# Optimization experiments

Measured on AMD Instinct MI355X. Metric: run time of the kernel, lower is better.

Reference implementation:

```python
import jax, jax.numpy as jnp
import numpy as np

B, N, D = 4, 2048, 768
OUT = 768

def setup_inputs() -> dict:
    key = jax.random.key(0)
    k1, k2 = jax.random.split(key)
    x = jax.random.normal(k1, (B, N, D), dtype=jnp.float32)
    kernel = jax.random.normal(k2, (3, D, OUT), dtype=jnp.float32) * 0.02
    return {"x": x, "kernel": kernel}

def reference(x, kernel):
    # Single-head attention with shared QKV kernel stack [3, D, OUT]
    q = jnp.einsum('bnd,do->bno', x, kernel[0])
    k = jnp.einsum('bnd,do->bno', x, kernel[1])
    v = jnp.einsum('bnd,do->bno', x, kernel[2])
    # NOTE: original divides by 64**0.5 == 8 regardless of dims (faithful)
    scores = jnp.einsum('bqo,bko->bqk', q, k) / 8.0
    attn = jax.nn.softmax(scores, axis=-1)
    return jnp.einsum('bqk,bko->bqo', attn, v)
```

## Files before the change

kernel.cpp:

```cpp
#include <hip/hip_runtime.h>
#include <hip/hip_bf16.h>

constexpr int B_ = 4, N_ = 2048, D_ = 768, OUT_ = 768;
constexpr int M_ = B_ * N_;

typedef __attribute__((ext_vector_type(8))) short short8;
typedef __attribute__((ext_vector_type(4))) float floatx4;

__device__ __forceinline__ unsigned short f2bfu(float f) {
    union { __hip_bfloat16 b; unsigned short u; } cv;
    cv.b = __float2bfloat16(f);
    return cv.u;
}

#define GLOAD_LDS16(g, l)                                                     \
    __builtin_amdgcn_global_load_lds(                                         \
        (const __attribute__((address_space(1))) void*)(g),                   \
        (__attribute__((address_space(3))) void*)(l), 16, 0, 0)

template <int NT>
__device__ __forceinline__ void gemm256_core(
    const __hip_bfloat16* __restrict__ aG, int lda,
    const __hip_bfloat16* __restrict__ bG, int ldb,
    unsigned short* LDS, floatx4 (&acc)[8][4]) {
    const int tid = threadIdx.x;
    const int wave = tid >> 6, lane = tid & 63;
    const int lrow = lane & 15, kq = lane >> 4;
    const int wm = (wave >> 2) * 128, wn = (wave & 3) * 64;

    const __hip_bfloat16* sA[2];
    const __hip_bfloat16* sB[2];
#pragma unroll
    for (int i = 0; i < 2; ++i) {
        const int u = i * 512 + tid;
        const int p = u >> 3, g = (u & 7) ^ (p & 7);
        const int row = 2 * p + (g >> 2), ch = g & 3;
        sA[i] = aG + (size_t)row * lda + ch * 8;
        sB[i] = bG + (size_t)row * ldb + ch * 8;
    }
    int offA[8], offB[4];
#pragma unroll
    for (int mi = 0; mi < 8; ++mi) {
        const int row = wm + mi * 16 + lrow;
        const int p = row >> 1, g = ((row & 1) << 2) | kq;
        offA[mi] = p * 64 + ((g ^ (p & 7)) * 8);
    }
#pragma unroll
    for (int ni = 0; ni < 4; ++ni) {
        const int row = wn + ni * 16 + lrow;
        const int p = row >> 1, g = ((row & 1) << 2) | kq;
        offB[ni] = p * 64 + ((g ^ (p & 7)) * 8);
    }

#define STAGE_T(ti)                                                        \
    do {                                                                   \
        unsigned short* dst_ = LDS + ((ti) & 3) * 16384 + wave * 512;      \
        GLOAD_LDS16(sA[0], dst_);                                          \
        GLOAD_LDS16(sA[1], dst_ + 4096);                                   \
        GLOAD_LDS16(sB[0], dst_ + 8192);                                   \
        GLOAD_LDS16(sB[1], dst_ + 12288);                                  \
        sA[0] += 32; sA[1] += 32; sB[0] += 32; sB[1] += 32;                \
    } while (0)

    STAGE_T(0);
    STAGE_T(1);
    STAGE_T(2);
    asm volatile("s_waitcnt vmcnt(8)" ::: "memory");
    __builtin_amdgcn_s_barrier();
    __builtin_amdgcn_sched_barrier(0);

    for (int t = 0; t < NT; ++t) {
        if (t + 3 < NT) STAGE_T(t + 3);
        const unsigned short* Sa = LDS + (t & 3) * 16384;
        const unsigned short* Sb = Sa + 8192;
        short8 bf[4], af[8];
#pragma unroll
        for (int ni = 0; ni < 4; ++ni)
            bf[ni] = *(const short8*)(Sb + offB[ni]);
#pragma unroll
        for (int mi = 0; mi < 8; ++mi)
            af[mi] = *(const short8*)(Sa + offA[mi]);
        __builtin_amdgcn_s_setprio(1);
#pragma unroll
        for (int mi = 0; mi < 8; ++mi)
#pragma unroll
            for (int ni = 0; ni < 4; ++ni)
                acc[mi][ni] = __builtin_amdgcn_mfma_f32_16x16x32_bf16(
                    af[mi], bf[ni], acc[mi][ni], 0, 0, 0);
        __builtin_amdgcn_s_setprio(0);
        if (t + 3 < NT) {
            asm volatile("s_waitcnt vmcnt(8)" ::: "memory");
        } else if (t + 2 < NT) {
            asm volatile("s_waitcnt vmcnt(4)" ::: "memory");
        } else if (t + 1 < NT) {
            asm volatile("s_waitcnt vmcnt(0)" ::: "memory");
        }
        if (t + 1 < NT) {
            __builtin_amdgcn_s_barrier();
            __builtin_amdgcn_sched_barrier(0);
        }
    }
#undef STAGE_T
}

__global__ __launch_bounds__(256)
void prep(const float* __restrict__ x, const float* __restrict__ w,
          __hip_bfloat16* __restrict__ xb, __hip_bfloat16* __restrict__ wt,
          float* __restrict__ l, float* __restrict__ out) {
    __shared__ float t[32][33];
    const int tid = threadIdx.x;
    if (blockIdx.x < 3072) {
        const size_t i = (size_t)blockIdx.x * 2048 + (size_t)tid * 8;
        float4 a = *(const float4*)(x + i);
        float4 b = *(const float4*)(x + i + 4);
        *(ushort4*)((unsigned short*)xb + i) =
            make_ushort4(f2bfu(a.x), f2bfu(a.y), f2bfu(a.z), f2bfu(a.w));
        *(ushort4*)((unsigned short*)xb + i + 4) =
            make_ushort4(f2bfu(b.x), f2bfu(b.y), f2bfu(b.z), f2bfu(b.w));
    } else if (blockIdx.x < 4800) {
        const int bid = blockIdx.x - 3072;
        const int s = bid / 576, rem = bid % 576;
        const int d0 = (rem / 24) * 32, o0 = (rem % 24) * 32;
        const int tx = tid & 31, ty = tid >> 5;
        const float* ws = w + (size_t)s * D_ * OUT_;
        __hip_bfloat16* wts = wt + (size_t)s * OUT_ * D_;
#pragma unroll
        for (int i = 0; i < 4; ++i)
            t[ty + 8 * i][tx] = ws[(size_t)(d0 + ty + 8 * i) * OUT_ + o0 + tx];
        __syncthreads();
#pragma unroll
        for (int i = 0; i < 4; ++i)
            wts[(size_t)(o0 + ty + 8 * i) * D_ + d0 + tx] =
                __float2bfloat16(t[tx][ty + 8 * i]);
    } else if (blockIdx.x == 4800) {
        float4* l4 = (float4*)l;
#pragma unroll
        for (int i = 0; i < 8; ++i) l4[i * 256 + tid] = make_float4(0, 0, 0, 0);
    } else {
        const size_t bid2 = blockIdx.x - 4801;
        ((float4*)out)[bid2 * 256 + tid] = make_float4(0, 0, 0, 0);
    }
}

__global__ __launch_bounds__(512, 2)
void qkv_mfma(const __hip_bfloat16* __restrict__ xb,
              const __hip_bfloat16* __restrict__ wt,
              __hip_bfloat16* __restrict__ q, __hip_bfloat16* __restrict__ k,
              __hip_bfloat16* __restrict__ vt) {
    __shared__ __align__(16) unsigned short LDS[65536];
    const int s = blockIdx.z;
    const int m0 = blockIdx.x * 256, n0 = blockIdx.y * 256;
    floatx4 acc[8][4] = {};
    gemm256_core<24>(xb + (size_t)m0 * D_, D_,
                     wt + (size_t)s * OUT_ * D_ + (size_t)n0 * D_, D_, LDS,
                     acc);

    const int tid = threadIdx.x, wave = tid >> 6, lane = tid & 63;
    const int lrow = lane & 15, kq = lane >> 4;
    const int wm = (wave >> 2) * 128, wn = (wave & 3) * 64;

    if (s < 2) {
        unsigned short* outp = (unsigned short*)(s == 0 ? q : k);
#pragma unroll
        for (int mi = 0; mi < 8; ++mi)
#pragma unroll
            for (int r = 0; r < 4; ++r) {
                const size_t ro =
                    (size_t)(m0 + wm + mi * 16 + kq * 4 + r) * OUT_ + n0 + wn;
#pragma unroll
                for (int ni = 0; ni < 4; ++ni)
                    outp[ro + ni * 16 + lrow] = f2bfu(acc[mi][ni][r]);
            }
    } else {
        unsigned short* E = LDS;
        const int b = m0 >> 11, j0 = m0 & 2047;
#pragma unroll
        for (int h = 0; h < 2; ++h) {
            __syncthreads();
            if ((wave >> 2) == h) {
#pragma unroll
                for (int ni = 0; ni < 4; ++ni)
#pragma unroll
                    for (int mi = 0; mi < 8; ++mi)
#pragma unroll
                        for (int r = 0; r < 4; ++r)
                            E[(wn + ni * 16 + lrow) * 136 + mi * 16 + kq * 4 +
                              r] = f2bfu(acc[mi][ni][r]);
            }
            __syncthreads();
#pragma unroll
            for (int i = 0; i < 8; ++i) {
                const int u = i * 512 + tid, nr = u >> 4, c = u & 15;
                short8 vv = *(const short8*)(E + nr * 136 + c * 8);
                *(short8*)((unsigned short*)vt +
                           ((size_t)b * OUT_ + n0 + nr) * N_ + j0 + h * 128 +
                           c * 8) = vv;
            }
        }
    }
}

__global__ __launch_bounds__(512, 2)
void scores_mfma(const __hip_bfloat16* __restrict__ q,
                 const __hip_bfloat16* __restrict__ k,
                 __hip_bfloat16* __restrict__ pt, float* __restrict__ l) {
    __shared__ __align__(16) unsigned short LDS[65536];
    const int b = blockIdx.z;
    const int m0 = blockIdx.x * 256, n0 = blockIdx.y * 256;
    floatx4 acc[8][4] = {};
    gemm256_core<24>(q + (size_t)b * N_ * OUT_ + (size_t)m0 * OUT_, OUT_,
                     k + (size_t)b * N_ * OUT_ + (size_t)n0 * OUT_, OUT_, LDS,
                     acc);

    const int tid = threadIdx.x, wave = tid >> 6, lane = tid & 63;
    const int lrow = lane & 15, kq = lane >> 4;
    const int wm = (wave >> 2) * 128, wn = (wave & 3) * 64;

    float rs[8][4];
#pragma unroll
    for (int mi = 0; mi < 8; ++mi)
#pragma unroll
        for (int r = 0; r < 4; ++r) rs[mi][r] = 0.0f;
#pragma unroll
    for (int mi = 0; mi < 8; ++mi)
#pragma unroll
        for (int ni = 0; ni < 4; ++ni)
#pragma unroll
            for (int r = 0; r < 4; ++r) {
                const float e = __expf(acc[mi][ni][r] * 0.125f - 8.0f);
                acc[mi][ni][r] = e;
                rs[mi][r] += e;
            }
#pragma unroll
    for (int mi = 0; mi < 8; ++mi)
#pragma unroll
        for (int r = 0; r < 4; ++r) {
            float v = rs[mi][r];
            v += __shfl_xor(v, 1, 64);
            v += __shfl_xor(v, 2, 64);
            v += __shfl_xor(v, 4, 64);
            v += __shfl_xor(v, 8, 64);
            if (lrow == 0)
                atomicAdd(&l[(size_t)b * N_ + m0 + wm + mi * 16 + kq * 4 + r],
                          v);
        }
    unsigned short* pb = (unsigned short*)pt + (size_t)b * N_ * N_;
#pragma unroll
    for (int mi = 0; mi < 8; ++mi)
#pragma unroll
        for (int r = 0; r < 4; ++r) {
            const size_t ro =
                (size_t)(m0 + wm + mi * 16 + kq * 4 + r) * N_ + n0 + wn;
#pragma unroll
            for (int ni = 0; ni < 4; ++ni)
                pb[ro + ni * 16 + lrow] = f2bfu(acc[mi][ni][r]);
        }
}

__global__ __launch_bounds__(512, 2)
void pv_mfma(const __hip_bfloat16* __restrict__ pt,
             const __hip_bfloat16* __restrict__ vt,
             const float* __restrict__ l, float* __restrict__ out) {
    __shared__ __align__(16) unsigned short LDS[65536];
    const int b = blockIdx.z >> 1, h = blockIdx.z & 1;
    const int m0 = blockIdx.x * 256, n0 = blockIdx.y * 256;
    floatx4 acc[8][4] = {};
    gemm256_core<32>(
        pt + (size_t)b * N_ * N_ + (size_t)m0 * N_ + h * 1024, N_,
        vt + (size_t)b * OUT_ * N_ + (size_t)n0 * N_ + h * 1024, N_, LDS, acc);

    const int tid = threadIdx.x, wave = tid >> 6, lane = tid & 63;
    const int lrow = lane & 15, kq = lane >> 4;
    const int wm = (wave >> 2) * 128, wn = (wave & 3) * 64;
    const float* lb = l + (size_t)b * N_ + m0 + wm;
#pragma unroll
    for (int mi = 0; mi < 8; ++mi)
#pragma unroll
        for (int r = 0; r < 4; ++r) {
            const float inv = 1.0f / lb[mi * 16 + kq * 4 + r];
            float* o = out +
                       ((size_t)b * N_ + m0 + wm + mi * 16 + kq * 4 + r) *
                           OUT_ +
                       n0 + wn;
#pragma unroll
            for (int ni = 0; ni < 4; ++ni)
                atomicAdd(o + ni * 16 + lrow, acc[mi][ni][r] * inv);
        }
}

extern "C" void kernel_launch(void* const* d_in, const int* in_sizes, int n_in,
                              void* d_out, int out_size, void* d_ws,
                              size_t ws_size, hipStream_t stream) {
    const float* x = (const float*)d_in[0];
    const float* w = (const float*)d_in[1];
    float* out = (float*)d_out;

    __hip_bfloat16* q  = (__hip_bfloat16*)d_ws;
    __hip_bfloat16* k  = q + (size_t)M_ * OUT_;
    __hip_bfloat16* vt = k + (size_t)M_ * OUT_;
    __hip_bfloat16* xb = vt + (size_t)M_ * OUT_;
    __hip_bfloat16* wt = xb + (size_t)M_ * D_;
    float* l = (float*)(wt + (size_t)3 * OUT_ * D_);
    __hip_bfloat16* pt = (__hip_bfloat16*)(l + M_);

    prep<<<dim3(10945), dim3(256), 0, stream>>>(x, w, xb, wt, l, out);
    qkv_mfma<<<dim3(32, 3, 3), dim3(512), 0, stream>>>(xb, wt, q, k, vt);
    scores_mfma<<<dim3(8, 8, 4), dim3(512), 0, stream>>>(q, k, pt, l);
    pv_mfma<<<dim3(8, 3, 8), dim3(512), 0, stream>>>(pt, vt, l, out);
}
```

Baseline: 227.5 us.

## Restructure GEMM pipelines with 64-wide K double-buffering and smaller M tiles

Replaces the shared 256x256 GEMM core with two variants that stage a 64-wide K step in two halves with double buffering: a 256x256 version for scores and a 128x256 version for the QKV and PV products. The 128x256 tile doubles the block count for QKV and PV. PV no longer splits K, so its output is written with plain stores instead of atomics and the output-zeroing pass in prep is removed. Q/K and score epilogues are staged through LDS to produce 16-byte coalesced stores. The price is more barriers per K step and a different LDS footprint.

```diff
diff --git a/kernel.cpp b/kernel.cpp
--- a/kernel.cpp
+++ b/kernel.cpp
@@ -18,95 +18,236 @@
         (const __attribute__((address_space(1))) void*)(g),                   \
         (__attribute__((address_space(3))) void*)(l), 16, 0, 0)
 
+#define MFMA_BF16 __builtin_amdgcn_mfma_f32_16x16x32_bf16
+#define WAIT_LGKM0 asm volatile("s_waitcnt lgkmcnt(0)" ::: "memory")
+
+
 template <int NT>
-__device__ __forceinline__ void gemm256_core(
+__device__ __forceinline__ void gemm4p(
     const __hip_bfloat16* __restrict__ aG, int lda,
     const __hip_bfloat16* __restrict__ bG, int ldb,
     unsigned short* LDS, floatx4 (&acc)[8][4]) {
+    constexpr int ASLOT = 8192, BSLOT = 8192, BUFS = 32768;
     const int tid = threadIdx.x;
     const int wave = tid >> 6, lane = tid & 63;
     const int lrow = lane & 15, kq = lane >> 4;
     const int wm = (wave >> 2) * 128, wn = (wave & 3) * 64;
 
-    const __hip_bfloat16* sA[2];
-    const __hip_bfloat16* sB[2];
-#pragma unroll
-    for (int i = 0; i < 2; ++i) {
-        const int u = i * 512 + tid;
-        const int p = u >> 3, g = (u & 7) ^ (p & 7);
-        const int row = 2 * p + (g >> 2), ch = g & 3;
-        sA[i] = aG + (size_t)row * lda + ch * 8;
-        sB[i] = bG + (size_t)row * ldb + ch * 8;
-    }
-    int offA[8], offB[4];
-#pragma unroll
-    for (int mi = 0; mi < 8; ++mi) {
-        const int row = wm + mi * 16 + lrow;
-        const int p = row >> 1, g = ((row & 1) << 2) | kq;
-        offA[mi] = p * 64 + ((g ^ (p & 7)) * 8);
-    }
-#pragma unroll
-    for (int ni = 0; ni < 4; ++ni) {
-        const int row = wn + ni * 16 + lrow;
-        const int p = row >> 1, g = ((row & 1) << 2) | kq;
-        offB[ni] = p * 64 + ((g ^ (p & 7)) * 8);
-    }
-
-#define STAGE_T(ti)                                                        \
-    do {                                                                   \
-        unsigned short* dst_ = LDS + ((ti) & 3) * 16384 + wave * 512;      \
-        GLOAD_LDS16(sA[0], dst_);                                          \
-        GLOAD_LDS16(sA[1], dst_ + 4096);                                   \
-        GLOAD_LDS16(sB[0], dst_ + 8192);                                   \
-        GLOAD_LDS16(sB[1], dst_ + 12288);                                  \
-        sA[0] += 32; sA[1] += 32; sB[0] += 32; sB[1] += 32;                \
+    const __hip_bfloat16 *sa0, *sa1, *sb0, *sb1;
+    {
+        const int r0 = tid >> 2, g0 = (tid & 3) ^ (r0 & 3);
+        sa0 = aG + (size_t)r0 * lda + g0 * 8;
+        sb0 = bG + (size_t)r0 * ldb + g0 * 8;
+        const int u1 = 512 + tid, r1 = u1 >> 2, g1 = (u1 & 3) ^ (r1 & 3);
+        sa1 = aG + (size_t)r1 * lda + g1 * 8;
+        sb1 = bG + (size_t)r1 * ldb + g1 * 8;
+    }
+    int oa[8], ob[4];
+#pragma unroll
+    for (int i = 0; i < 8; ++i) {
+        const int r = wm + i * 16 + lrow;
+        oa[i] = r * 32 + ((kq ^ (r & 3)) * 8);
+    }
+#pragma unroll
+    for (int i = 0; i < 4; ++i) {
+        const int r = wn + i * 16 + lrow;
+        ob[i] = r * 32 + ((kq ^ (r & 3)) * 8);
+    }
+
+#define SA4(tt, kh)                                                          \
+    do {                                                                     \
+        unsigned short* d_ =                                                 \
+            LDS + ((tt) & 1) * BUFS + (kh) * ASLOT + wave * 512;             \
+        GLOAD_LDS16(sa0 + (tt) * 64 + (kh) * 32, d_);                        \
+        GLOAD_LDS16(sa1 + (tt) * 64 + (kh) * 32, d_ + 4096);                 \
     } while (0)
-
-    STAGE_T(0);
-    STAGE_T(1);
-    STAGE_T(2);
-    asm volatile("s_waitcnt vmcnt(8)" ::: "memory");
+#define SB4(tt, kh)                                                          \
+    do {                                                                     \
+        unsigned short* d_ = LDS + ((tt) & 1) * BUFS + 2 * ASLOT +           \
+                             (kh) * BSLOT + wave * 512;                      \
+        GLOAD_LDS16(sb0 + (tt) * 64 + (kh) * 32, d_);                        \
+        GLOAD_LDS16(sb1 + (tt) * 64 + (kh) * 32, d_ + 4096);                 \
+    } while (0)
+
+    SA4(0, 0); SB4(0, 0); SA4(0, 1); SB4(0, 1);
+    SA4(1, 0); SB4(1, 0); SA4(1, 1);
+    asm volatile("s_waitcnt vmcnt(6)" ::: "memory");
     __builtin_amdgcn_s_barrier();
     __builtin_amdgcn_sched_barrier(0);
 
     for (int t = 0; t < NT; ++t) {
-        if (t + 3 < NT) STAGE_T(t + 3);
-        const unsigned short* Sa = LDS + (t & 3) * 16384;
-        const unsigned short* Sb = Sa + 8192;
-        short8 bf[4], af[8];
-#pragma unroll
-        for (int ni = 0; ni < 4; ++ni)
-            bf[ni] = *(const short8*)(Sb + offB[ni]);
-#pragma unroll
-        for (int mi = 0; mi < 8; ++mi)
-            af[mi] = *(const short8*)(Sa + offA[mi]);
-        __builtin_amdgcn_s_setprio(1);
-#pragma unroll
-        for (int mi = 0; mi < 8; ++mi)
+        const unsigned short* Ab = LDS + (t & 1) * BUFS;
+        const unsigned short* Bb = Ab + 2 * ASLOT;
+        short8 af[8], bf0, bf1;
+#pragma unroll
+        for (int i = 0; i < 8; ++i) af[i] = *(const short8*)(Ab + oa[i]);
+        bf0 = *(const short8*)(Bb + ob[0]);
+        bf1 = *(const short8*)(Bb + ob[1]);
+        if (t + 1 < NT) SB4(t + 1, 1);
+        __builtin_amdgcn_s_barrier();
+        WAIT_LGKM0;
+        __builtin_amdgcn_sched_barrier(0);
+        __builtin_amdgcn_s_setprio(1);
+#pragma unroll
+        for (int mi = 0; mi < 8; ++mi) {
+            acc[mi][0] = MFMA_BF16(af[mi], bf0, acc[mi][0], 0, 0, 0);
+            acc[mi][1] = MFMA_BF16(af[mi], bf1, acc[mi][1], 0, 0, 0);
+        }
+        __builtin_amdgcn_s_setprio(0);
+        __builtin_amdgcn_s_barrier();
+        bf0 = *(const short8*)(Bb + ob[2]);
+        bf1 = *(const short8*)(Bb + ob[3]);
+        if (t + 2 < NT) SA4(t + 2, 0);
+        __builtin_amdgcn_s_barrier();
+        WAIT_LGKM0;
+        __builtin_amdgcn_sched_barrier(0);
+        __builtin_amdgcn_s_setprio(1);
+#pragma unroll
+        for (int mi = 0; mi < 8; ++mi) {
+            acc[mi][2] = MFMA_BF16(af[mi], bf0, acc[mi][2], 0, 0, 0);
+            acc[mi][3] = MFMA_BF16(af[mi], bf1, acc[mi][3], 0, 0, 0);
+        }
+        __builtin_amdgcn_s_setprio(0);
+        __builtin_amdgcn_s_barrier();
+#pragma unroll
+        for (int i = 0; i < 8; ++i)
+            af[i] = *(const short8*)(Ab + ASLOT + oa[i]);
+        bf0 = *(const short8*)(Bb + BSLOT + ob[2]);
+        bf1 = *(const short8*)(Bb + BSLOT + ob[3]);
+        if (t + 2 < NT) SB4(t + 2, 0);
+        __builtin_amdgcn_s_barrier();
+        WAIT_LGKM0;
+        __builtin_amdgcn_sched_barrier(0);
+        __builtin_amdgcn_s_setprio(1);
+#pragma unroll
+        for (int mi = 0; mi < 8; ++mi) {
+            acc[mi][2] = MFMA_BF16(af[mi], bf0, acc[mi][2], 0, 0, 0);
+            acc[mi][3] = MFMA_BF16(af[mi], bf1, acc[mi][3], 0, 0, 0);
+        }
+        __builtin_amdgcn_s_setprio(0);
+        __builtin_amdgcn_s_barrier();
+        bf0 = *(const short8*)(Bb + BSLOT + ob[0]);
+        bf1 = *(const short8*)(Bb + BSLOT + ob[1]);
+        if (t + 2 < NT) SA4(t + 2, 1);
+        __builtin_amdgcn_s_barrier();
+        WAIT_LGKM0;
+        __builtin_amdgcn_sched_barrier(0);
+        __builtin_amdgcn_s_setprio(1);
+#pragma unroll
+        for (int mi = 0; mi < 8; ++mi) {
+            acc[mi][0] = MFMA_BF16(af[mi], bf0, acc[mi][0], 0, 0, 0);
+            acc[mi][1] = MFMA_BF16(af[mi], bf1, acc[mi][1], 0, 0, 0);
+        }
+        __builtin_amdgcn_s_setprio(0);
+        if (t + 2 < NT)
+            asm volatile("s_waitcnt vmcnt(6)" ::: "memory");
+        else if (t + 1 < NT)
+            asm volatile("s_waitcnt vmcnt(0)" ::: "memory");
+        __builtin_amdgcn_s_barrier();
+        __builtin_amdgcn_sched_barrier(0);
+    }
+#undef SA4
+#undef SB4
+}
+
+template <int NT>
+__device__ __forceinline__ void gemm2p(
+    const __hip_bfloat16* __restrict__ aG, int lda,
+    const __hip_bfloat16* __restrict__ bG, int ldb,
+    unsigned short* LDS, floatx4 (&acc)[4][4]) {
+    constexpr int ASLOT = 4096, BSLOT = 8192, BUFS = 24576;
+    const int tid = threadIdx.x;
+    const int wave = tid >> 6, lane = tid & 63;
+    const int lrow = lane & 15, kq = lane >> 4;
+    const int wm = (wave >> 2) * 64, wn = (wave & 3) * 64;
+
+    const __hip_bfloat16 *sa0, *sb0, *sb1;
+    {
+        const int r0 = tid >> 2, g0 = (tid & 3) ^ (r0 & 3);
+        sa0 = aG + (size_t)r0 * lda + g0 * 8;
+        sb0 = bG + (size_t)r0 * ldb + g0 * 8;
+        const int u1 = 512 + tid, r1 = u1 >> 2, g1 = (u1 & 3) ^ (r1 & 3);
+        sb1 = bG + (size_t)r1 * ldb + g1 * 8;
+    }
+    int oa[4], ob[4];
+#pragma unroll
+    for (int i = 0; i < 4; ++i) {
+        const int ra = wm + i * 16 + lrow;
+        oa[i] = ra * 32 + ((kq ^ (ra & 3)) * 8);
+        const int rb = wn + i * 16 + lrow;
+        ob[i] = rb * 32 + ((kq ^ (rb & 3)) * 8);
+    }
+
+#define SA2(tt, kh)                                                          \
+    GLOAD_LDS16(sa0 + (tt) * 64 + (kh) * 32,                                 \
+                LDS + ((tt) & 1) * BUFS + (kh) * ASLOT + wave * 512)
+#define SB2(tt, kh)                                                          \
+    do {                                                                     \
+        unsigned short* d_ = LDS + ((tt) & 1) * BUFS + 2 * ASLOT +           \
+                             (kh) * BSLOT + wave * 512;                      \
+        GLOAD_LDS16(sb0 + (tt) * 64 + (kh) * 32, d_);                        \
+        GLOAD_LDS16(sb1 + (tt) * 64 + (kh) * 32, d_ + 4096);                 \
+    } while (0)
+
+    SA2(0, 0); SB2(0, 0);
+    SA2(0, 1); SB2(0, 1);
+    SA2(1, 0); SB2(1, 0);
+    asm volatile("s_waitcnt vmcnt(3)" ::: "memory");
+    __builtin_amdgcn_s_barrier();
+    __builtin_amdgcn_sched_barrier(0);
+
+    for (int t = 0; t < NT; ++t) {
+        const unsigned short* Ab = LDS + (t & 1) * BUFS;
+        const unsigned short* Bb = Ab + 2 * ASLOT;
+        short8 af[4], bf[4];
+#pragma unroll
+        for (int i = 0; i < 4; ++i) af[i] = *(const short8*)(Ab + oa[i]);
+#pragma unroll
+        for (int i = 0; i < 4; ++i) bf[i] = *(const short8*)(Bb + ob[i]);
+        if (t + 1 < NT) { SA2(t + 1, 1); SB2(t + 1, 1); }
+        __builtin_amdgcn_s_barrier();
+        WAIT_LGKM0;
+        __builtin_amdgcn_sched_barrier(0);
+        __builtin_amdgcn_s_setprio(1);
+#pragma unroll
+        for (int mi = 0; mi < 4; ++mi)
 #pragma unroll
             for (int ni = 0; ni < 4; ++ni)
-                acc[mi][ni] = __builtin_amdgcn_mfma_f32_16x16x32_bf16(
-                    af[mi], bf[ni], acc[mi][ni], 0, 0, 0);
-        __builtin_amdgcn_s_setprio(0);
-        if (t + 3 < NT) {
-            asm volatile("s_waitcnt vmcnt(8)" ::: "memory");
-        } else if (t + 2 < NT) {
-            asm volatile("s_waitcnt vmcnt(4)" ::: "memory");
-        } else if (t + 1 < NT) {
+                acc[mi][ni] = MFMA_BF16(af[mi], bf[ni], acc[mi][ni], 0, 0, 0);
+        __builtin_amdgcn_s_setprio(0);
+        __builtin_amdgcn_s_barrier();
+#pragma unroll
+        for (int i = 0; i < 4; ++i)
+            af[i] = *(const short8*)(Ab + ASLOT + oa[i]);
+#pragma unroll
+        for (int i = 0; i < 4; ++i)
+            bf[i] = *(const short8*)(Bb + BSLOT + ob[i]);
+        if (t + 2 < NT) { SA2(t + 2, 0); SB2(t + 2, 0); }
+        __builtin_amdgcn_s_barrier();
+        WAIT_LGKM0;
+        __builtin_amdgcn_sched_barrier(0);
+        __builtin_amdgcn_s_setprio(1);
+#pragma unroll
+        for (int mi = 0; mi < 4; ++mi)
+#pragma unroll
+            for (int ni = 0; ni < 4; ++ni)
+                acc[mi][ni] = MFMA_BF16(af[mi], bf[ni], acc[mi][ni], 0, 0, 0);
+        __builtin_amdgcn_s_setprio(0);
+        if (t + 2 < NT)
+            asm volatile("s_waitcnt vmcnt(3)" ::: "memory");
+        else if (t + 1 < NT)
             asm volatile("s_waitcnt vmcnt(0)" ::: "memory");
-        }
-        if (t + 1 < NT) {
-            __builtin_amdgcn_s_barrier();
-            __builtin_amdgcn_sched_barrier(0);
-        }
-    }
-#undef STAGE_T
+        __builtin_amdgcn_s_barrier();
+        __builtin_amdgcn_sched_barrier(0);
+    }
+#undef SA2
+#undef SB2
 }
 
 __global__ __launch_bounds__(256)
 void prep(const float* __restrict__ x, const float* __restrict__ w,
           __hip_bfloat16* __restrict__ xb, __hip_bfloat16* __restrict__ wt,
-          float* __restrict__ l, float* __restrict__ out) {
+          float* __restrict__ l) {
     __shared__ float t[32][33];
     const int tid = threadIdx.x;
     if (blockIdx.x < 3072) {
@@ -132,13 +273,10 @@
         for (int i = 0; i < 4; ++i)
             wts[(size_t)(o0 + ty + 8 * i) * D_ + d0 + tx] =
                 __float2bfloat16(t[tx][ty + 8 * i]);
-    } else if (blockIdx.x == 4800) {
+    } else {
         float4* l4 = (float4*)l;
 #pragma unroll
         for (int i = 0; i < 8; ++i) l4[i * 256 + tid] = make_float4(0, 0, 0, 0);
-    } else {
-        const size_t bid2 = blockIdx.x - 4801;
-        ((float4*)out)[bid2 * 256 + tid] = make_float4(0, 0, 0, 0);
     }
 }
 
@@ -147,55 +285,57 @@
               const __hip_bfloat16* __restrict__ wt,
               __hip_bfloat16* __restrict__ q, __hip_bfloat16* __restrict__ k,
               __hip_bfloat16* __restrict__ vt) {
-    __shared__ __align__(16) unsigned short LDS[65536];
+    __shared__ __align__(16) unsigned short LDS[49152];
     const int s = blockIdx.z;
-    const int m0 = blockIdx.x * 256, n0 = blockIdx.y * 256;
-    floatx4 acc[8][4] = {};
-    gemm256_core<24>(xb + (size_t)m0 * D_, D_,
-                     wt + (size_t)s * OUT_ * D_ + (size_t)n0 * D_, D_, LDS,
-                     acc);
+    const int m0 = blockIdx.x * 128, n0 = blockIdx.y * 256;
+    floatx4 acc[4][4] = {};
+    gemm2p<12>(xb + (size_t)m0 * D_, D_,
+               wt + (size_t)s * OUT_ * D_ + (size_t)n0 * D_, D_, LDS, acc);
 
     const int tid = threadIdx.x, wave = tid >> 6, lane = tid & 63;
     const int lrow = lane & 15, kq = lane >> 4;
-    const int wm = (wave >> 2) * 128, wn = (wave & 3) * 64;
+    const int wm = (wave >> 2) * 64, wn = (wave & 3) * 64;
+    unsigned short* E = LDS;
 
     if (s < 2) {
+        __syncthreads();
+#pragma unroll
+        for (int mi = 0; mi < 4; ++mi)
+#pragma unroll
+            for (int ni = 0; ni < 4; ++ni) {
+                const int n = wn + ni * 16 + lrow;
+#pragma unroll
+                for (int r = 0; r < 4; ++r)
+                    E[(wm + mi * 16 + kq * 4 + r) * 264 + n] =
+                        f2bfu(acc[mi][ni][r]);
+            }
+        __syncthreads();
         unsigned short* outp = (unsigned short*)(s == 0 ? q : k);
 #pragma unroll
-        for (int mi = 0; mi < 8; ++mi)
-#pragma unroll
-            for (int r = 0; r < 4; ++r) {
-                const size_t ro =
-                    (size_t)(m0 + wm + mi * 16 + kq * 4 + r) * OUT_ + n0 + wn;
-#pragma unroll
-                for (int ni = 0; ni < 4; ++ni)
-                    outp[ro + ni * 16 + lrow] = f2bfu(acc[mi][ni][r]);
+        for (int i = 0; i < 8; ++i) {
+            const int u = i * 512 + tid, row = u >> 5, c = u & 31;
+            *(short8*)(outp + (size_t)(m0 + row) * OUT_ + n0 + c * 8) =
+                *(const short8*)(E + row * 264 + c * 8);
+        }
+    } else {
+        __syncthreads();
+#pragma unroll
+        for (int mi = 0; mi < 4; ++mi)
+#pragma unroll
+            for (int ni = 0; ni < 4; ++ni) {
+                const int n = wn + ni * 16 + lrow;
+#pragma unroll
+                for (int r = 0; r < 4; ++r)
+                    E[n * 136 + wm + mi * 16 + kq * 4 + r] =
+                        f2bfu(acc[mi][ni][r]);
             }
-    } else {
-        unsigned short* E = LDS;
+        __syncthreads();
         const int b = m0 >> 11, j0 = m0 & 2047;
 #pragma unroll
-        for (int h = 0; h < 2; ++h) {
-            __syncthreads();
-            if ((wave >> 2) == h) {
-#pragma unroll
-                for (int ni = 0; ni < 4; ++ni)
-#pragma unroll
-                    for (int mi = 0; mi < 8; ++mi)
-#pragma unroll
-                        for (int r = 0; r < 4; ++r)
-                            E[(wn + ni * 16 + lrow) * 136 + mi * 16 + kq * 4 +
-                              r] = f2bfu(acc[mi][ni][r]);
-            }
-            __syncthreads();
-#pragma unroll
-            for (int i = 0; i < 8; ++i) {
-                const int u = i * 512 + tid, nr = u >> 4, c = u & 15;
-                short8 vv = *(const short8*)(E + nr * 136 + c * 8);
-                *(short8*)((unsigned short*)vt +
-                           ((size_t)b * OUT_ + n0 + nr) * N_ + j0 + h * 128 +
-                           c * 8) = vv;
-            }
+        for (int i = 0; i < 8; ++i) {
+            const int u = i * 512 + tid, nr = u >> 4, c = u & 15;
+            *(short8*)((unsigned short*)vt + ((size_t)b * OUT_ + n0 + nr) * N_ +
+                       j0 + c * 8) = *(const short8*)(E + nr * 136 + c * 8);
         }
     }
 }
@@ -208,9 +348,8 @@
     const int b = blockIdx.z;
     const int m0 = blockIdx.x * 256, n0 = blockIdx.y * 256;
     floatx4 acc[8][4] = {};
-    gemm256_core<24>(q + (size_t)b * N_ * OUT_ + (size_t)m0 * OUT_, OUT_,
-                     k + (size_t)b * N_ * OUT_ + (size_t)n0 * OUT_, OUT_, LDS,
-                     acc);
+    gemm4p<12>(q + (size_t)b * N_ * OUT_ + (size_t)m0 * OUT_, OUT_,
+               k + (size_t)b * N_ * OUT_ + (size_t)n0 * OUT_, OUT_, LDS, acc);
 
     const int tid = threadIdx.x, wave = tid >> 6, lane = tid & 63;
     const int lrow = lane & 15, kq = lane >> 4;
@@ -244,37 +383,51 @@
                 atomicAdd(&l[(size_t)b * N_ + m0 + wm + mi * 16 + kq * 4 + r],
                           v);
         }
+
+    unsigned short* E = LDS;
     unsigned short* pb = (unsigned short*)pt + (size_t)b * N_ * N_;
 #pragma unroll
-    for (int mi = 0; mi < 8; ++mi)
-#pragma unroll
-        for (int r = 0; r < 4; ++r) {
-            const size_t ro =
-                (size_t)(m0 + wm + mi * 16 + kq * 4 + r) * N_ + n0 + wn;
-#pragma unroll
-            for (int ni = 0; ni < 4; ++ni)
-                pb[ro + ni * 16 + lrow] = f2bfu(acc[mi][ni][r]);
-        }
+    for (int h = 0; h < 2; ++h) {
+        __syncthreads();
+        if ((wave >> 2) == h) {
+#pragma unroll
+            for (int mi = 0; mi < 8; ++mi)
+#pragma unroll
+                for (int ni = 0; ni < 4; ++ni) {
+                    const int n = wn + ni * 16 + lrow;
+#pragma unroll
+                    for (int r = 0; r < 4; ++r)
+                        E[(mi * 16 + kq * 4 + r) * 258 + n] =
+                            f2bfu(acc[mi][ni][r]);
+                }
+        }
+        __syncthreads();
+#pragma unroll
+        for (int i = 0; i < 8; ++i) {
+            const int u = i * 512 + tid, row = u >> 5, c = u & 31;
+            *(short8*)(pb + (size_t)(m0 + h * 128 + row) * N_ + n0 + c * 8) =
+                *(const short8*)(E + row * 258 + c * 8);
+        }
+    }
 }
 
 __global__ __launch_bounds__(512, 2)
 void pv_mfma(const __hip_bfloat16* __restrict__ pt,
              const __hip_bfloat16* __restrict__ vt,
              const float* __restrict__ l, float* __restrict__ out) {
-    __shared__ __align__(16) unsigned short LDS[65536];
-    const int b = blockIdx.z >> 1, h = blockIdx.z & 1;
-    const int m0 = blockIdx.x * 256, n0 = blockIdx.y * 256;
-    floatx4 acc[8][4] = {};
-    gemm256_core<32>(
-        pt + (size_t)b * N_ * N_ + (size_t)m0 * N_ + h * 1024, N_,
-        vt + (size_t)b * OUT_ * N_ + (size_t)n0 * N_ + h * 1024, N_, LDS, acc);
+    __shared__ __align__(16) unsigned short LDS[49152];
+    const int b = blockIdx.z;
+    const int m0 = blockIdx.x * 128, n0 = blockIdx.y * 256;
+    floatx4 acc[4][4] = {};
+    gemm2p<32>(pt + (size_t)b * N_ * N_ + (size_t)m0 * N_, N_,
+               vt + (size_t)b * OUT_ * N_ + (size_t)n0 * N_, N_, LDS, acc);
 
     const int tid = threadIdx.x, wave = tid >> 6, lane = tid & 63;
     const int lrow = lane & 15, kq = lane >> 4;
-    const int wm = (wave >> 2) * 128, wn = (wave & 3) * 64;
+    const int wm = (wave >> 2) * 64, wn = (wave & 3) * 64;
     const float* lb = l + (size_t)b * N_ + m0 + wm;
 #pragma unroll
-    for (int mi = 0; mi < 8; ++mi)
+    for (int mi = 0; mi < 4; ++mi)
 #pragma unroll
         for (int r = 0; r < 4; ++r) {
             const float inv = 1.0f / lb[mi * 16 + kq * 4 + r];
@@ -284,7 +437,7 @@
                        n0 + wn;
 #pragma unroll
             for (int ni = 0; ni < 4; ++ni)
-                atomicAdd(o + ni * 16 + lrow, acc[mi][ni][r] * inv);
+                o[ni * 16 + lrow] = acc[mi][ni][r] * inv;
         }
 }
 
@@ -303,8 +456,8 @@
     float* l = (float*)(wt + (size_t)3 * OUT_ * D_);
     __hip_bfloat16* pt = (__hip_bfloat16*)(l + M_);
 
-    prep<<<dim3(10945), dim3(256), 0, stream>>>(x, w, xb, wt, l, out);
-    qkv_mfma<<<dim3(32, 3, 3), dim3(512), 0, stream>>>(xb, wt, q, k, vt);
+    prep<<<dim3(4801), dim3(256), 0, stream>>>(x, w, xb, wt, l);
+    qkv_mfma<<<dim3(64, 3, 3), dim3(512), 0, stream>>>(xb, wt, q, k, vt);
     scores_mfma<<<dim3(8, 8, 4), dim3(512), 0, stream>>>(q, k, pt, l);
-    pv_mfma<<<dim3(8, 3, 8), dim3(512), 0, stream>>>(pt, vt, l, out);
-}
+    pv_mfma<<<dim3(16, 3, 4), dim3(512), 0, stream>>>(pt, vt, l, out);
+}
```

Measured after the change: 201.5 us. 1.13x faster.
